# Performance work log

Measured on AMD Instinct MI355X. Metric: run time of the kernel, lower is better.

Reference implementation:

```python
import jax, jax.numpy as jnp
import numpy as np

N, P, T, D = 25000, 100000, 4, 128
DIN = 4 * D + 4  # 516
LEAKY = 0.001


def setup_inputs() -> dict:
    key = jax.random.key(0)
    ks = jax.random.split(key, 12)
    inp = {
        "coords": jax.random.normal(ks[0], (N, T, 3), jnp.float32),
        "propers": jax.random.randint(ks[1], (P, 4), 0, N, jnp.int64),
        "encoded": jax.random.normal(ks[2], (N, D), jnp.float32),
        "t": jax.random.uniform(ks[3], (T,), jnp.float32),
        "answer": jax.random.normal(ks[4], (N, T, 3), jnp.float32),
        # AggregateMLP(516 -> 128 -> 128 -> 128 -> 2), LeakyReLU(0.001) between
        "W0": jax.random.normal(ks[5], (DIN, D), jnp.float32) / np.sqrt(DIN),
        "b0": jnp.zeros((D,), jnp.float32),
        "W1": jax.random.normal(ks[6], (D, D), jnp.float32) / np.sqrt(D),
        "b1": jnp.zeros((D,), jnp.float32),
        "W2": jax.random.normal(ks[7], (D, D), jnp.float32) / np.sqrt(D),
        "b2": jnp.zeros((D,), jnp.float32),
        "W3": jax.random.normal(ks[8], (D, 2), jnp.float32) / np.sqrt(D),
        "b3": jnp.zeros((2,), jnp.float32),
    }
    return inp


def _forward(coords, propers, encoded, t, answer, W0, b0, W1, b1, W2, b2, W3, b3):
    p0, p1, p2, p3 = propers[:, 0], propers[:, 1], propers[:, 2], propers[:, 3]
    c0, c1, c2, c3 = coords[p0], coords[p1], coords[p2], coords[p3]  # [P,T,3]
    u1 = c1 - c0
    u2 = c2 - c1
    u3 = c3 - c2
    u1xu2 = jnp.cross(u1, u2, axis=-1)
    u2xu3 = jnp.cross(u2, u3, axis=-1)
    u2_norm = jnp.linalg.norm(u2, axis=-1, keepdims=True)
    u1yu2 = u1 * u2_norm
    theta = jnp.arctan2((u1yu2 * u2xu3).sum(-1), (u1xu2 * u2xu3).sum(-1))  # [P,T]
    dr = c0 - c3  # [P,T,3]
    dl = jnp.sqrt(jnp.clip(jnp.square(dr).sum(-1), 1e-12))  # [P,T]
    dh = dr / dl[..., None]

    Pn, Tn = propers.shape[0], t.shape[0]
    bcast = lambda e: jnp.broadcast_to(e[:, None, :], (Pn, Tn, e.shape[-1]))
    feats = jnp.concatenate(
        [
            bcast(encoded[p0]),
            bcast(encoded[p1]),
            bcast(encoded[p2]),
            bcast(encoded[p3]),
            jnp.broadcast_to(t.reshape(1, Tn, 1), (Pn, Tn, 1)),
            jnp.sin(theta)[..., None],
            jnp.cos(theta)[..., None],
            dl[..., None],
        ],
        axis=2,
    )  # [P,T,516]

    h = jax.nn.leaky_relu(feats @ W0 + b0, LEAKY)
    h = jax.nn.leaky_relu(h @ W1 + b1, LEAKY)
    h = jax.nn.leaky_relu(h @ W2 + b2, LEAKY)
    delta = h @ W3 + b3  # [P,T,2]

    out = answer.at[p0].add(-0.5 * delta[:, :, 0:1] * dh)
    out = out.at[p3].add(0.5 * delta[:, :, 1:2] * dh)
    return out


def reference(coords, propers, encoded, t, answer, W0, b0, W1, b1, W2, b2, W3, b3):
    return _forward(coords, propers, encoded, t, answer, W0, b0, W1, b1, W2, b2, W3, b3)
```

## Files before the change

### kernel.cpp

```cpp
#include <hip/hip_runtime.h>
#include <hip/hip_bf16.h>

#define NN 25000
#define PP 100000
#define TT 4
#define DD 128
#define LEAKY 0.001f

#define PB 32
#define ROWS 128

typedef __bf16 bf16;
typedef __bf16 bf16x8 __attribute__((ext_vector_type(8)));
typedef float  f32x4  __attribute__((ext_vector_type(4)));

#define OFF_W0SW  0u
#define OFF_W1SW  131072u
#define OFF_W2SW  163840u
#define OFF_W3SW  196608u
#define OFF_WTB   200704u
#define OFF_W5B   201728u
#define OFF_E     202496u
#define WS_END    25802496u

#define PR_W0SW  8192
#define PR_W1SW  2048
#define PR_W2SW  2048
#define PR_W3SW  256
#define PR_WTB   64
#define PR_W5B   48
#define PR_COPY4 75000
#define PR_TOTAL (PR_W0SW + PR_W1SW + PR_W2SW + PR_W3SW + PR_WTB + PR_W5B + PR_COPY4)

#define LGKM0() asm volatile("s_waitcnt lgkmcnt(0)" ::: "memory")

__device__ __forceinline__ void gload_lds16(const void* g, void* l) {
    __builtin_amdgcn_global_load_lds(
        (const __attribute__((address_space(1))) void*)g,
        (__attribute__((address_space(3))) void*)l, 16, 0, 0);
}

__global__ __launch_bounds__(256) void prep_kernel(
    const float* __restrict__ W0, const float* __restrict__ W1,
    const float* __restrict__ W2, const float* __restrict__ W3,
    const float* __restrict__ answer, const float* __restrict__ tvec,
    const float* __restrict__ b0,
    bf16* __restrict__ W0sw, bf16* __restrict__ W1sw, bf16* __restrict__ W2sw,
    bf16* __restrict__ W3sw, bf16* __restrict__ WtB, bf16* __restrict__ W5B,
    float* __restrict__ out)
{
    int idx = blockIdx.x * 256 + threadIdx.x;
    if (idx < PR_W0SW) {
        int lane = idx & 63, c = idx >> 6;
        int fr = lane & 15, quad = lane >> 4;
        int kc = c & 15, iwv = c >> 4;
        bf16 v[8];
        #pragma unroll
        for (int j = 0; j < 8; ++j)
            v[j] = (bf16)W0[(kc * 32 + quad * 8 + j) * 128 + iwv * 16 + fr];
        *(bf16x8*)(W0sw + c * 512 + lane * 8) = *(const bf16x8*)v;
        return;
    }
    idx -= PR_W0SW;
    if (idx < PR_W1SW) {
        int lane = idx & 63, c = idx >> 6;
        int fr = lane & 15, quad = lane >> 4;
        int kc = c & 3, nt = c >> 2;
        bf16 v[8];
        #pragma unroll
        for (int j = 0; j < 8; ++j)
            v[j] = (bf16)W1[(kc * 32 + quad * 8 + j) * 128 + nt * 16 + fr];
        *(bf16x8*)(W1sw + c * 512 + lane * 8) = *(const bf16x8*)v;
        return;
    }
    idx -= PR_W1SW;
    if (idx < PR_W2SW) {
        int lane = idx & 63, c = idx >> 6;
        int fr = lane & 15, quad = lane >> 4;
        int kc = c & 3, nt = c >> 2;
        bf16 v[8];
        #pragma unroll
        for (int j = 0; j < 8; ++j)
            v[j] = (bf16)W2[(kc * 32 + quad * 8 + j) * 128 + nt * 16 + fr];
        *(bf16x8*)(W2sw + c * 512 + lane * 8) = *(const bf16x8*)v;
        return;
    }
    idx -= PR_W2SW;
    if (idx < PR_W3SW) {
        int lane = idx & 63, kc = idx >> 6;
        int fr = lane & 15, quad = lane >> 4;
        bf16 v[8];
        #pragma unroll
        for (int j = 0; j < 8; ++j)
            v[j] = (fr < 2) ? (bf16)W3[(kc * 32 + quad * 8 + j) * 2 + fr] : (bf16)0.0f;
        *(bf16x8*)(W3sw + kc * 512 + lane * 8) = *(const bf16x8*)v;
        return;
    }
    idx -= PR_W3SW;
    if (idx < PR_WTB) {
        int t = idx >> 4, s = idx & 15;
        float tv = tvec[t];
        bf16 v[8];
        #pragma unroll
        for (int j = 0; j < 8; ++j)
            v[j] = (bf16)(tv * W0[512 * 128 + s * 8 + j] + b0[s * 8 + j]);
        *(bf16x8*)(WtB + t * 128 + s * 8) = *(const bf16x8*)v;
        return;
    }
    idx -= PR_WTB;
    if (idx < PR_W5B) {
        int r = idx >> 4, s = idx & 15;
        bf16 v[8];
        #pragma unroll
        for (int j = 0; j < 8; ++j)
            v[j] = (bf16)W0[(513 + r) * 128 + s * 8 + j];
        *(bf16x8*)(W5B + r * 128 + s * 8) = *(const bf16x8*)v;
        return;
    }
    idx -= PR_W5B;
    if (idx < PR_COPY4) { ((float4*)out)[idx] = ((const float4*)answer)[idx]; }
}

__global__ __launch_bounds__(256) void prep_e_kernel(
    const float* __restrict__ encoded, const bf16* __restrict__ W0sw,
    bf16* __restrict__ E)
{
    __shared__ bf16 sA[64][136];
    __shared__ bf16 sT[64][40];
    const int tid = threadIdx.x;
    const int row0 = (blockIdx.x >> 2) * 64;
    const int ntb  = blockIdx.x & 3;
    for (int c = tid; c < 2048; c += 256) {
        int row = c >> 5, seg = c & 31;
        int rr = row0 + row; if (rr >= NN) rr = NN - 1;
        float4 v = *(const float4*)(encoded + (size_t)rr * 128 + seg * 4);
        bf16 pk[4] = {(bf16)v.x, (bf16)v.y, (bf16)v.z, (bf16)v.w};
        *(uint2*)(&sA[row][seg * 4]) = *(const uint2*)pk;
    }
    __syncthreads();
    const int wv = tid >> 6, lane = tid & 63;
    const int fr = lane & 15, quad = lane >> 4;
    const bf16* aBase = &sA[wv * 16 + fr][quad * 8];
    bf16x8 aFv[4];
    #pragma unroll
    for (int kcc = 0; kcc < 4; ++kcc) aFv[kcc] = *(const bf16x8*)(aBase + kcc * 32);
    const int orow = tid >> 2, oseg = tid & 3;
    #pragma unroll
    for (int i = 0; i < 4; ++i) {
        #pragma unroll
        for (int ntl = 0; ntl < 2; ++ntl) {
            int nt = ntb * 2 + ntl;
            f32x4 acc = {0.f, 0.f, 0.f, 0.f};
            #pragma unroll
            for (int kcc = 0; kcc < 4; ++kcc) {
                bf16x8 bF = *(const bf16x8*)(W0sw + ((size_t)nt * 16 + i * 4 + kcc) * 512 + lane * 8);
                acc = __builtin_amdgcn_mfma_f32_16x16x32_bf16(aFv[kcc], bF, acc, 0, 0, 0);
            }
            #pragma unroll
            for (int reg = 0; reg < 4; ++reg)
                sT[wv * 16 + quad * 4 + reg][ntl * 16 + fr] = (bf16)acc[reg];
        }
        LGKM0();
        bf16x8 ev = *(const bf16x8*)(&sT[orow][oseg * 8]);
        LGKM0();
        if (row0 + orow < NN)
            *(bf16x8*)(E + ((size_t)i * NN + row0 + orow) * 128 + ntb * 32 + oseg * 8) = ev;
    }
}

__global__ __launch_bounds__(512, 4) void main_kernel(
    const float* __restrict__ coords, const int* __restrict__ propers,
    const float* __restrict__ b1, const float* __restrict__ b2,
    const float* __restrict__ b3,
    const bf16* __restrict__ E, const bf16* __restrict__ W1sw,
    const bf16* __restrict__ W2sw, const bf16* __restrict__ W3sw,
    const bf16* __restrict__ WtB, const bf16* __restrict__ W5B,
    float* __restrict__ out)
{
    __shared__ __align__(16) bf16 sH[8][16][136];
    __shared__ __align__(16) bf16 sW[18432];
    __shared__ float sScr[8][16][6];
    __shared__ int   sNd[8][8];

    const int tid  = threadIdx.x;
    const int wv   = tid >> 6, lane = tid & 63;
    const int fr   = lane & 15, quad = lane >> 4;
    const int pw   = blockIdx.x * PB + wv * 4;

    {
        const char* g1 = (const char*)W1sw;
        char* l = (char*)&sW[0];
        #pragma unroll
        for (int r2 = 0; r2 < 4; ++r2)
            gload_lds16(g1 + r2 * 8192 + wv * 1024 + lane * 16,
                        l + r2 * 8192 + wv * 1024);
        if (wv < 4)
            gload_lds16((const char*)W3sw + wv * 1024 + lane * 16,
                        l + 32768 + wv * 1024);
    }

    int4 pv = *(const int4*)(propers + (size_t)(pw + quad) * 4);
    bf16x8 e0 = *(const bf16x8*)(E + ((size_t)0 * NN + pv.x) * 128 + fr * 8);
    bf16x8 e1 = *(const bf16x8*)(E + ((size_t)1 * NN + pv.y) * 128 + fr * 8);
    bf16x8 e2 = *(const bf16x8*)(E + ((size_t)2 * NN + pv.z) * 128 + fr * 8);
    bf16x8 e3 = *(const bf16x8*)(E + ((size_t)3 * NN + pv.w) * 128 + fr * 8);
    if (fr == 0) { sNd[wv][quad * 2] = pv.x; sNd[wv][quad * 2 + 1] = pv.w; }
    bf16x8 w3v = *(const bf16x8*)(W5B + 0 * 128 + fr * 8);
    bf16x8 w4v = *(const bf16x8*)(W5B + 1 * 128 + fr * 8);
    bf16x8 w5v = *(const bf16x8*)(W5B + 2 * 128 + fr * 8);

    float b1r[8], b2r[8];
    #pragma unroll
    for (int i = 0; i < 8; ++i) {
        b1r[i] = b1[i * 16 + fr];
        b2r[i] = b2[i * 16 + fr];
    }
    float b3r = (fr < 2) ? b3[fr] : 0.0f;

    float snl = 0.f, csl = 1.f, dll = 0.f;
    if (lane < 16) {
        int pp_ = lane >> 2, t = lane & 3;
        int4 pg = *(const int4*)(propers + (size_t)(pw + pp_) * 4);
        const float* c0 = coords + (size_t)pg.x * 12 + t * 3;
        const float* c1 = coords + (size_t)pg.y * 12 + t * 3;
        const float* c2 = coords + (size_t)pg.z * 12 + t * 3;
        const float* c3 = coords + (size_t)pg.w * 12 + t * 3;
        float u1x = c1[0]-c0[0], u1y = c1[1]-c0[1], u1z = c1[2]-c0[2];
        float u2x = c2[0]-c1[0], u2y = c2[1]-c1[1], u2z = c2[2]-c1[2];
        float u3x = c3[0]-c2[0], u3y = c3[1]-c2[1], u3z = c3[2]-c2[2];
        float ax = u1y*u2z - u1z*u2y, ay = u1z*u2x - u1x*u2z, az = u1x*u2y - u1y*u2x;
        float bx = u2y*u3z - u2z*u3y, by = u2z*u3x - u2x*u3z, bz = u2x*u3y - u2y*u3x;
        float u2n = sqrtf(u2x*u2x + u2y*u2y + u2z*u2z);
        float num = u2n * (u1x*bx + u1y*by + u1z*bz);
        float den = ax*bx + ay*by + az*bz;
        float hyp = sqrtf(num*num + den*den);
        if (hyp > 1e-30f) { float ih = 1.0f / hyp; snl = num * ih; csl = den * ih; }
        else { snl = 0.0f; csl = 1.0f; }
        float drx = c0[0]-c3[0], dry = c0[1]-c3[1], drz = c0[2]-c3[2];
        dll = sqrtf(fmaxf(drx*drx + dry*dry + drz*drz, 1e-12f));
        float il = 1.0f / dll;
        sScr[wv][lane][0] = drx * il;
        sScr[wv][lane][1] = dry * il;
        sScr[wv][lane][2] = drz * il;
    }

    {
        float g[8], w3f[8], w4f[8], w5f[8];
        #pragma unroll
        for (int j = 0; j < 8; ++j) {
            g[j]   = (float)e0[j] + (float)e1[j] + (float)e2[j] + (float)e3[j];
            w3f[j] = (float)w3v[j]; w4f[j] = (float)w4v[j]; w5f[j] = (float)w5v[j];
        }
        #pragma unroll
        for (int t = 0; t < 4; ++t) {
            int r = quad * 4 + t;
            bf16x8 wtv = *(const bf16x8*)(WtB + t * 128 + fr * 8);
            float sn = __shfl(snl, r), cs = __shfl(csl, r), dl = __shfl(dll, r);
            bf16 hv[8];
            #pragma unroll
            for (int j = 0; j < 8; ++j) {
                float v = g[j] + (float)wtv[j] + sn * w3f[j] + cs * w4f[j] + dl * w5f[j];
                v = fmaxf(v, LEAKY * v);
                hv[j] = (bf16)v;
            }
            *(bf16x8*)(&sH[wv][r][fr * 8]) = *(const bf16x8*)hv;
        }
    }
    __syncthreads();

#define DENSE_LAYER(BR)                                                         \
    {                                                                           \
        LGKM0();            \
        bf16x8 aF[4];                                                           \
        const bf16* aRow = &sH[wv][fr][quad * 8];                               \
        _Pragma("unroll")                                                       \
        for (int kc = 0; kc < 4; ++kc)                                          \
            aF[kc] = *(const bf16x8*)(aRow + kc * 32);                          \
        LGKM0();      \
        _Pragma("unroll")                                                       \
        for (int hh = 0; hh < 2; ++hh) {                                        \
            f32x4 acc[4];                                                       \
            _Pragma("unroll")                                                   \
            for (int nt = 0; nt < 4; ++nt) acc[nt] = (f32x4){0.f,0.f,0.f,0.f};  \
            _Pragma("unroll")                                                   \
            for (int kc = 0; kc < 4; ++kc) {                                    \
                _Pragma("unroll")                                               \
                for (int nt = 0; nt < 4; ++nt) {                                \
                    bf16x8 bF = *(const bf16x8*)(sW +                           \
                        ((hh * 4 + nt) * 4 + kc) * 512 + lane * 8);             \
                    acc[nt] = __builtin_amdgcn_mfma_f32_16x16x32_bf16(          \
                        aF[kc], bF, acc[nt], 0, 0, 0);                          \
                }                                                               \
            }                                                                   \
            _Pragma("unroll")                                                   \
            for (int nt = 0; nt < 4; ++nt) {                                    \
                int j = (hh * 4 + nt) * 16 + fr;                                \
                float bb = BR[hh * 4 + nt];                                     \
                _Pragma("unroll")                                               \
                for (int reg = 0; reg < 4; ++reg) {                             \
                    float v = acc[nt][reg] + bb;                                \
                    v = fmaxf(v, LEAKY * v);                                    \
                    sH[wv][quad * 4 + reg][j] = (bf16)v;                        \
                }                                                               \
            }                                                                   \
        }                                                                       \
    }

    DENSE_LAYER(b1r)
    __syncthreads();
    {
        const char* g2 = (const char*)W2sw;
        char* l = (char*)&sW[0];
        #pragma unroll
        for (int r2 = 0; r2 < 4; ++r2)
            gload_lds16(g2 + r2 * 8192 + wv * 1024 + lane * 16,
                        l + r2 * 8192 + wv * 1024);
    }
    __syncthreads();
    DENSE_LAYER(b2r)

    {
        LGKM0();
        bf16x8 aF[4];
        const bf16* aRow = &sH[wv][fr][quad * 8];
        #pragma unroll
        for (int kc = 0; kc < 4; ++kc)
            aF[kc] = *(const bf16x8*)(aRow + kc * 32);
        f32x4 dacc = {0.f, 0.f, 0.f, 0.f};
        #pragma unroll
        for (int kc = 0; kc < 4; ++kc) {
            bf16x8 bF = *(const bf16x8*)(sW + 16384 + kc * 512 + lane * 8);
            dacc = __builtin_amdgcn_mfma_f32_16x16x32_bf16(aF[kc], bF, dacc, 0, 0, 0);
        }
        if (fr < 2) {
            #pragma unroll
            for (int reg = 0; reg < 4; ++reg)
                sScr[wv][quad * 4 + reg][3 + fr] = dacc[reg] + b3r;
        }
    }

    LGKM0();
    for (int idx = lane; idx < 96; idx += 64) {
        int r = idx / 6, c = idx - (idx / 6) * 6;
        int side = c / 3, ax = c - side * 3;
        int node = sNd[wv][(r >> 2) * 2 + side];
        float dval = (side ? 0.5f : -0.5f) * sScr[wv][r][3 + side];
        atomicAdd(out + (size_t)node * 12 + (r & 3) * 3 + ax, dval * sScr[wv][r][ax]);
    }
#undef DENSE_LAYER
}

extern "C" void kernel_launch(void* const* d_in, const int* in_sizes, int n_in,
                              void* d_out, int out_size, void* d_ws, size_t ws_size,
                              hipStream_t stream) {
    const float* coords  = (const float*)d_in[0];
    const int*   propers = (const int*)d_in[1];
    const float* encoded = (const float*)d_in[2];
    const float* tvec    = (const float*)d_in[3];
    const float* answer  = (const float*)d_in[4];
    const float* W0 = (const float*)d_in[5];
    const float* b0 = (const float*)d_in[6];
    const float* W1 = (const float*)d_in[7];
    const float* b1 = (const float*)d_in[8];
    const float* W2 = (const float*)d_in[9];
    const float* b2 = (const float*)d_in[10];
    const float* W3 = (const float*)d_in[11];
    const float* b3 = (const float*)d_in[12];
    float* out = (float*)d_out;
    char* ws = (char*)d_ws;
    bf16* W0sw = (bf16*)(ws + OFF_W0SW);
    bf16* W1sw = (bf16*)(ws + OFF_W1SW);
    bf16* W2sw = (bf16*)(ws + OFF_W2SW);
    bf16* W3sw = (bf16*)(ws + OFF_W3SW);
    bf16* WtB  = (bf16*)(ws + OFF_WTB);
    bf16* W5B  = (bf16*)(ws + OFF_W5B);
    bf16* E    = (bf16*)(ws + OFF_E);

    int prep_blocks = (PR_TOTAL + 255) / 256;
    prep_kernel<<<prep_blocks, 256, 0, stream>>>(W0, W1, W2, W3, answer, tvec, b0,
                                                 W0sw, W1sw, W2sw, W3sw, WtB, W5B, out);
    prep_e_kernel<<<391 * 4, 256, 0, stream>>>(encoded, W0sw, E);
    main_kernel<<<PP / PB, 512, 0, stream>>>(coords, propers, b1, b2, b3,
                                             E, W1sw, W2sw, W3sw, WtB, W5B, out);
}
```

Before: 167.0 us.

## Pack FP32 math into 2-wide vectors, add MFMA priority, drop LDS waits, restructure atomics

New measurement: 166.5 us (median of 2 runs). About the same (-0.3%).

```diff
diff --git a/kernel.cpp b/kernel.cpp
--- a/kernel.cpp
+++ b/kernel.cpp
@@ -13,6 +13,7 @@
 typedef __bf16 bf16;
 typedef __bf16 bf16x8 __attribute__((ext_vector_type(8)));
 typedef float  f32x4  __attribute__((ext_vector_type(4)));
+typedef float  f32x2  __attribute__((ext_vector_type(2)));
 
 #define OFF_W0SW  0u
 #define OFF_W1SW  131072u
@@ -245,23 +246,34 @@
     }
 
     {
-        float g[8], w3f[8], w4f[8], w5f[8];
-        #pragma unroll
-        for (int j = 0; j < 8; ++j) {
-            g[j]   = (float)e0[j] + (float)e1[j] + (float)e2[j] + (float)e3[j];
-            w3f[j] = (float)w3v[j]; w4f[j] = (float)w4v[j]; w5f[j] = (float)w5v[j];
+        f32x2 g2[4], w3f2[4], w4f2[4], w5f2[4];
+        #pragma unroll
+        for (int j = 0; j < 4; ++j) {
+            g2[j] = (f32x2){
+                (float)e0[2*j]   + (float)e1[2*j]   + (float)e2[2*j]   + (float)e3[2*j],
+                (float)e0[2*j+1] + (float)e1[2*j+1] + (float)e2[2*j+1] + (float)e3[2*j+1] };
+            w3f2[j] = (f32x2){ (float)w3v[2*j], (float)w3v[2*j+1] };
+            w4f2[j] = (f32x2){ (float)w4v[2*j], (float)w4v[2*j+1] };
+            w5f2[j] = (f32x2){ (float)w5v[2*j], (float)w5v[2*j+1] };
         }
         #pragma unroll
         for (int t = 0; t < 4; ++t) {
             int r = quad * 4 + t;
             bf16x8 wtv = *(const bf16x8*)(WtB + t * 128 + fr * 8);
             float sn = __shfl(snl, r), cs = __shfl(csl, r), dl = __shfl(dll, r);
+            f32x2 sn2 = {sn, sn}, cs2 = {cs, cs}, dl2 = {dl, dl};
             bf16 hv[8];
             #pragma unroll
-            for (int j = 0; j < 8; ++j) {
-                float v = g[j] + (float)wtv[j] + sn * w3f[j] + cs * w4f[j] + dl * w5f[j];
-                v = fmaxf(v, LEAKY * v);
-                hv[j] = (bf16)v;
+            for (int j = 0; j < 4; ++j) {
+                f32x2 v = g2[j] + (f32x2){ (float)wtv[2*j], (float)wtv[2*j+1] };
+                v = sn2 * w3f2[j] + v;
+                v = cs2 * w4f2[j] + v;
+                v = dl2 * w5f2[j] + v;
+                f32x2 lv = v * LEAKY;
+                v.x = fmaxf(v.x, lv.x);
+                v.y = fmaxf(v.y, lv.y);
+                hv[2*j]   = (bf16)v.x;
+                hv[2*j+1] = (bf16)v.y;
             }
             *(bf16x8*)(&sH[wv][r][fr * 8]) = *(const bf16x8*)hv;
         }
@@ -270,18 +282,17 @@
 
 #define DENSE_LAYER(BR)                                                         \
     {                                                                           \
-        LGKM0();            \
         bf16x8 aF[4];                                                           \
         const bf16* aRow = &sH[wv][fr][quad * 8];                               \
         _Pragma("unroll")                                                       \
         for (int kc = 0; kc < 4; ++kc)                                          \
             aF[kc] = *(const bf16x8*)(aRow + kc * 32);                          \
-        LGKM0();      \
         _Pragma("unroll")                                                       \
         for (int hh = 0; hh < 2; ++hh) {                                        \
             f32x4 acc[4];                                                       \
             _Pragma("unroll")                                                   \
             for (int nt = 0; nt < 4; ++nt) acc[nt] = (f32x4){0.f,0.f,0.f,0.f};  \
+            __builtin_amdgcn_s_setprio(1);                                      \
             _Pragma("unroll")                                                   \
             for (int kc = 0; kc < 4; ++kc) {                                    \
                 _Pragma("unroll")                                               \
@@ -292,16 +303,17 @@
                         aF[kc], bF, acc[nt], 0, 0, 0);                          \
                 }                                                               \
             }                                                                   \
+            __builtin_amdgcn_s_setprio(0);                                      \
             _Pragma("unroll")                                                   \
             for (int nt = 0; nt < 4; ++nt) {                                    \
                 int j = (hh * 4 + nt) * 16 + fr;                                \
-                float bb = BR[hh * 4 + nt];                                     \
+                f32x4 v = acc[nt] + BR[hh * 4 + nt];                            \
+                f32x4 lv = v * LEAKY;                                           \
+                v.x = fmaxf(v.x, lv.x); v.y = fmaxf(v.y, lv.y);                 \
+                v.z = fmaxf(v.z, lv.z); v.w = fmaxf(v.w, lv.w);                 \
                 _Pragma("unroll")                                               \
-                for (int reg = 0; reg < 4; ++reg) {                             \
-                    float v = acc[nt][reg] + bb;                                \
-                    v = fmaxf(v, LEAKY * v);                                    \
-                    sH[wv][quad * 4 + reg][j] = (bf16)v;                        \
-                }                                                               \
+                for (int reg = 0; reg < 4; ++reg)                               \
+                    sH[wv][quad * 4 + reg][j] = (bf16)v[reg];                   \
             }                                                                   \
         }                                                                       \
     }
@@ -320,18 +332,19 @@
     DENSE_LAYER(b2r)
 
     {
-        LGKM0();
         bf16x8 aF[4];
         const bf16* aRow = &sH[wv][fr][quad * 8];
         #pragma unroll
         for (int kc = 0; kc < 4; ++kc)
             aF[kc] = *(const bf16x8*)(aRow + kc * 32);
         f32x4 dacc = {0.f, 0.f, 0.f, 0.f};
+        __builtin_amdgcn_s_setprio(1);
         #pragma unroll
         for (int kc = 0; kc < 4; ++kc) {
             bf16x8 bF = *(const bf16x8*)(sW + 16384 + kc * 512 + lane * 8);
             dacc = __builtin_amdgcn_mfma_f32_16x16x32_bf16(aF[kc], bF, dacc, 0, 0, 0);
         }
+        __builtin_amdgcn_s_setprio(0);
         if (fr < 2) {
             #pragma unroll
             for (int reg = 0; reg < 4; ++reg)
@@ -339,13 +352,20 @@
         }
     }
 
-    LGKM0();
-    for (int idx = lane; idx < 96; idx += 64) {
-        int r = idx / 6, c = idx - (idx / 6) * 6;
-        int side = c / 3, ax = c - side * 3;
-        int node = sNd[wv][(r >> 2) * 2 + side];
-        float dval = (side ? 0.5f : -0.5f) * sScr[wv][r][3 + side];
-        atomicAdd(out + (size_t)node * 12 + (r & 3) * 3 + ax, dval * sScr[wv][r][ax]);
+    {
+        int row = lane & 15;
+        int comp = lane >> 4;
+        int side = (comp == 3) ? 1 : 0;
+        int ax = side ? 0 : comp;
+        int node = sNd[wv][(row >> 2) * 2 + side];
+        float dval = (side ? 0.5f : -0.5f) * sScr[wv][row][3 + side];
+        atomicAdd(out + (size_t)node * 12 + (row & 3) * 3 + ax, dval * sScr[wv][row][ax]);
+        if (lane < 32) {
+            int ax2 = 1 + comp;
+            int node2 = sNd[wv][(row >> 2) * 2 + 1];
+            float dval2 = 0.5f * sScr[wv][row][4];
+            atomicAdd(out + (size_t)node2 * 12 + (row & 3) * 3 + ax2, dval2 * sScr[wv][row][ax2]);
+        }
     }
 #undef DENSE_LAYER
 }
```
